# Kernel tuning notes

Hardware: AMD Instinct MI355X
Metric: run time of the kernel (lower is better)

## Reference

```python
import jax, jax.numpy as jnp
import numpy as np
import math

E = 256      # emb_size
H = 4        # num_heads
D = E // H   # head_dim
EXPLORE_SCALE = 0.5
EXPLOIT_SCALE = 0.5
TEMP_MIN = 0.5
TEMP_MAX = 2.0


def setup_inputs() -> dict:
    key = jax.random.key(0)
    ks = jax.random.split(key, 12)
    B, S = 4, 2048
    his_emb = jax.random.normal(ks[0], (B, S, E), dtype=jnp.float32)
    src_key_padding_mask = jax.random.randint(ks[1], (B, S), 0, 2) > 0
    explore = jax.random.uniform(ks[2], (B, S), dtype=jnp.float32)
    exploit = jax.random.uniform(ks[3], (B, S), dtype=jnp.float32)
    scale = 1.0 / math.sqrt(E)
    Wq = jax.random.normal(ks[4], (E, E), dtype=jnp.float32) * scale
    bq = jnp.zeros((E,), dtype=jnp.float32)
    Wk = jax.random.normal(ks[5], (E, E), dtype=jnp.float32) * scale
    bk = jnp.zeros((E,), dtype=jnp.float32)
    Wv = jax.random.normal(ks[6], (E, E), dtype=jnp.float32) * scale
    bv = jnp.zeros((E,), dtype=jnp.float32)
    Wo = jax.random.normal(ks[7], (E, E), dtype=jnp.float32) * scale
    bo = jnp.zeros((E,), dtype=jnp.float32)
    return {"his_emb": his_emb, "src_key_padding_mask": src_key_padding_mask,
            "explore": explore, "exploit": exploit,
            "Wq": Wq, "bq": bq, "Wk": Wk, "bk": bk,
            "Wv": Wv, "bv": bv, "Wo": Wo, "bo": bo}


def reference(his_emb, src_key_padding_mask, explore, exploit,
              Wq, bq, Wk, bk, Wv, bv, Wo, bo):
    B, S, _ = his_emb.shape
    # projections -> [B, H, S, D]
    q = (his_emb @ Wq + bq).reshape(B, S, H, D).transpose(0, 2, 1, 3)
    k = (his_emb @ Wk + bk).reshape(B, S, H, D).transpose(0, 2, 1, 3)
    v = (his_emb @ Wv + bv).reshape(B, S, H, D).transpose(0, 2, 1, 3)
    logits = jnp.einsum('bhqd,bhkd->bhqk', q, k) / math.sqrt(D)
    attn_mask = src_key_padding_mask[:, None, None, :]  # [B,1,1,S] over keys
    logits = jnp.where(attn_mask, -1e16, logits)
    # per-query dynamic temperature
    temp = 1.0 + EXPLORE_SCALE * explore - EXPLOIT_SCALE * exploit  # [B,S]
    temp = jnp.clip(temp, TEMP_MIN, TEMP_MAX)
    temp = jnp.where(src_key_padding_mask, 1.0, temp)
    logits = logits / temp[:, None, :, None]
    probs = jax.nn.softmax(logits, axis=-1)
    probs = jnp.where(attn_mask, 0.0, probs)
    probs = probs / jnp.maximum(probs.sum(axis=-1, keepdims=True), 1e-8)
    out = jnp.einsum('bhqk,bhkd->bhqd', probs, v)
    out = out.transpose(0, 2, 1, 3).reshape(B, S, E)
    out = out @ Wo + bo
    return jnp.where(src_key_padding_mask[:, :, None], 0.0, out)
```

## Files before the change

kernel.cpp:

```cpp
#include <hip/hip_runtime.h>
#include <math.h>

#define B_ 4
#define S_ 2048
#define E_ 256
#define H_ 4
#define D_ 64
#define NROW (B_*S_)
#define NCH 2
#define CHK (S_/NCH)
#define NT (CHK/64)
#define LOG2E 1.4426950408889634f
#define NFM  (-17.312340490667562f)

typedef __attribute__((ext_vector_type(8)))  short short8;
typedef __attribute__((ext_vector_type(4)))  float floatx4;
typedef __attribute__((ext_vector_type(16))) float floatx16;

__device__ __forceinline__ short f2bf(float f){
    union{float f; unsigned u;} x; x.f = f;
    unsigned r = x.u + 0x7fffu + ((x.u>>16)&1u);
    return (short)(r>>16);
}
__device__ __forceinline__ unsigned cvtpk(float a, float b){
    unsigned r; asm("v_cvt_pk_bf16_f32 %0, %1, %2" : "=v"(r) : "v"(a), "v"(b)); return r;
}

__global__ __launch_bounds__(256) void prep(
    const float* __restrict__ W0, const float* __restrict__ W1,
    const float* __restrict__ W2, const float* __restrict__ W3,
    const float* __restrict__ X,
    short* __restrict__ T0, short* __restrict__ T1,
    short* __restrict__ T2, short* __restrict__ T3,
    short* __restrict__ Xb)
{
    __shared__ float L[64][65];
    const int t = threadIdx.x;
    if (blockIdx.x >= 16){
        const int cid = (blockIdx.x - 16) + 128*blockIdx.y;
        const float4* src = (const float4*)(X + (size_t)cid*4096 + t*16);
        short8 o0, o1; float4 u;
        u = src[0]; o0[0]=f2bf(u.x); o0[1]=f2bf(u.y); o0[2]=f2bf(u.z); o0[3]=f2bf(u.w);
        u = src[1]; o0[4]=f2bf(u.x); o0[5]=f2bf(u.y); o0[6]=f2bf(u.z); o0[7]=f2bf(u.w);
        u = src[2]; o1[0]=f2bf(u.x); o1[1]=f2bf(u.y); o1[2]=f2bf(u.z); o1[3]=f2bf(u.w);
        u = src[3]; o1[4]=f2bf(u.x); o1[5]=f2bf(u.y); o1[6]=f2bf(u.z); o1[7]=f2bf(u.w);
        short* dst = Xb + (size_t)cid*4096 + t*16;
        *(short8*)dst = o0; *(short8*)(dst+8) = o1;
        return;
    }
    const float* W = blockIdx.y==0?W0: blockIdx.y==1?W1: blockIdx.y==2?W2:W3;
    short*       T = blockIdx.y==0?T0: blockIdx.y==1?T1: blockIdx.y==2?T2:T3;
    const int k0 = (blockIdx.x>>2)*64, n0 = (blockIdx.x&3)*64;
    {
        int r = t>>2, c0 = (t&3)*16;
        const float4* p = (const float4*)(W + (size_t)(k0+r)*E_ + n0 + c0);
        #pragma unroll
        for (int j=0;j<4;++j){
            float4 u = p[j];
            L[r][c0+4*j]=u.x; L[r][c0+4*j+1]=u.y; L[r][c0+4*j+2]=u.z; L[r][c0+4*j+3]=u.w;
        }
    }
    __syncthreads();
    {
        int n = t>>2, kk0 = (t&3)*16;
        short8 o0, o1;
        #pragma unroll
        for(int j=0;j<8;++j) o0[j] = f2bf(L[kk0+j][n]);
        #pragma unroll
        for(int j=0;j<8;++j) o1[j] = f2bf(L[kk0+8+j][n]);
        short* dst = T + (size_t)(n0+n)*E_ + k0 + kk0;
        *(short8*)dst = o0; *(short8*)(dst+8) = o1;
    }
}

__global__ __launch_bounds__(256) void qkv_gemm(
    const short* __restrict__ Xb,
    const short* __restrict__ Wtq, const float* __restrict__ bq,
    const short* __restrict__ Wtk, const float* __restrict__ bk,
    const short* __restrict__ Wtv, const float* __restrict__ bv,
    short* __restrict__ Q, short* __restrict__ K, short* __restrict__ Vt)
{
    const int z = blockIdx.z;
    const short* Wt   = z==0?Wtq: z==1?Wtk:Wtv;
    const float* bias = z==0?bq:  z==1?bk:bv;

    __shared__ __align__(16) short As[64][72];
    __shared__ __align__(16) short Bs[64][72];

    const int t=threadIdx.x, w=t>>6, lane=t&63, ln=lane&15, quad=lane>>4;
    const int m0 = blockIdx.y*64, n0 = blockIdx.x*64;

    floatx4 acc[4] = {};
    for (int kt=0; kt<E_; kt+=64){
        __syncthreads();
        {
            int r=t>>2, c0=(t&3)*16;
            const uint4* pa = (const uint4*)(Xb + (size_t)(m0+r)*E_ + kt + c0);
            *(uint4*)&As[r][c0] = pa[0]; *(uint4*)&As[r][c0+8] = pa[1];
            const uint4* pb = (const uint4*)(Wt + (size_t)(n0+r)*E_ + kt + c0);
            *(uint4*)&Bs[r][c0] = pb[0]; *(uint4*)&Bs[r][c0+8] = pb[1];
        }
        __syncthreads();
        short8 a0 = *(const short8*)&As[w*16+ln][quad*8];
        short8 a1 = *(const short8*)&As[w*16+ln][32+quad*8];
        #pragma unroll
        for (int c=0;c<4;++c){
            short8 b0 = *(const short8*)&Bs[c*16+ln][quad*8];
            short8 b1 = *(const short8*)&Bs[c*16+ln][32+quad*8];
            acc[c] = __builtin_amdgcn_mfma_f32_16x16x32_bf16(a0,b0,acc[c],0,0,0);
            acc[c] = __builtin_amdgcn_mfma_f32_16x16x32_bf16(a1,b1,acc[c],0,0,0);
        }
    }
    if (z<2){
        short* dst = z==0?Q:K;
        #pragma unroll
        for(int c=0;c<4;++c){
            int colg = n0 + c*16 + ln;
            float bia = bias[colg];
            #pragma unroll
            for(int reg=0;reg<4;++reg){
                int row = m0 + w*16 + quad*4 + reg;
                dst[(size_t)row*E_ + colg] = f2bf(acc[c][reg] + bia);
            }
        }
    } else {
        #pragma unroll
        for(int c=0;c<4;++c){
            int colg = n0 + c*16 + ln;
            int hx = colg>>6, d = colg&63;
            float bia = bias[colg];
            #pragma unroll
            for(int reg=0;reg<4;++reg){
                int row = m0 + w*16 + quad*4 + reg;
                int bb = row>>11, s = row&(S_-1);
                Vt[((size_t)((bb*H_+hx)*D_+d))*S_ + s] = f2bf(acc[c][reg] + bia);
            }
        }
    }
}

__global__ __launch_bounds__(256) void attn_mfma(
    const short* __restrict__ Qb, const short* __restrict__ Kb, const short* __restrict__ Vtb,
    const int* __restrict__ mask,
    const float* __restrict__ explore, const float* __restrict__ exploit,
    float* __restrict__ OP, float* __restrict__ Lb)
{
    const int bid = blockIdx.x + 16*blockIdx.y + 32*blockIdx.z;
    const int swz = (bid & 7)*64 + (bid >> 3);
    const int bx = swz & 15;
    const int ck = (swz >> 4) & 1;
    const int z  = swz >> 5;
    const int b = z >> 2, h = z & 3;
    const int q0 = bx*128;
    const int k0 = ck*CHK;

    const int t = threadIdx.x, w = t>>6, lane = t&63, l31 = lane&31, hi = lane>>5;

    __shared__ __align__(16) short Ks[2][64][72];
    __shared__ __align__(16) short Vs[2][64][72];
    __shared__ float mb[2][64];

    const int qbase = q0 + w*32;
    const int qg = qbase + l31;
    float tsc2;
    {
        float ex = explore[b*S_+qg], xp = exploit[b*S_+qg];
        float tmp = fminf(fmaxf(1.0f + 0.5f*ex - 0.5f*xp, 0.5f), 2.0f);
        if (mask[b*S_+qg]) tmp = 1.0f;
        tsc2 = LOG2E/(tmp*8.0f);
    }
    const size_t qrow = (size_t)(b*S_+qg)*E_ + h*D_ + hi*8;
    const short8 qf0 = *(const short8*)(Qb + qrow);
    const short8 qf1 = *(const short8*)(Qb + qrow + 16);
    const short8 qf2 = *(const short8*)(Qb + qrow + 32);
    const short8 qf3 = *(const short8*)(Qb + qrow + 48);

    floatx16 ofa = {}, ofb = {};
    float lacc = 0.0f;

    const int sr = t>>2, sc = (t&3)*16;
    const short* kgp = Kb  + (size_t)(b*S_)*E_ + h*D_ + sc;
    const short* vgp = Vtb + ((size_t)(b*H_+h)*D_ + sr)*S_;

    uint4 rk0, rk1, rv0, rv1; float mfv = 0.0f;
    {
        const uint4* gk = (const uint4*)(kgp + (size_t)(k0+sr)*E_);
        rk0 = gk[0]; rk1 = gk[1];
        const uint4* gv = (const uint4*)(vgp + k0 + sc);
        rv0 = gv[0]; rv1 = gv[1];
        if (t < 64) mfv = mask[b*S_ + k0 + t] ? -1e30f : NFM;
    }
    *(uint4*)&Ks[0][sr][sc] = rk0; *(uint4*)&Ks[0][sr][sc+8] = rk1;
    *(uint4*)&Vs[0][sr][sc] = rv0; *(uint4*)&Vs[0][sr][sc+8] = rv1;
    if (t < 64) mb[0][t] = mfv;
    {
        const uint4* gk = (const uint4*)(kgp + (size_t)(k0+64+sr)*E_);
        rk0 = gk[0]; rk1 = gk[1];
        const uint4* gv = (const uint4*)(vgp + k0 + 64 + sc);
        rv0 = gv[0]; rv1 = gv[1];
        if (t < 64) mfv = mask[b*S_ + k0 + 64 + t] ? -1e30f : NFM;
    }
    __syncthreads();

    int cur = 0;
    #pragma unroll 1
    for (int it = 0; it < NT; ++it){
        const short (*Kc)[72] = Ks[cur];
        const short (*Vc)[72] = Vs[cur];
        #pragma unroll
        for (int kg = 0; kg < 2; ++kg){
            floatx16 st = {};
            const short8 kf0 = *(const short8*)&Kc[kg*32+l31][hi*8];
            const short8 kf1 = *(const short8*)&Kc[kg*32+l31][16+hi*8];
            const short8 kf2 = *(const short8*)&Kc[kg*32+l31][32+hi*8];
            const short8 kf3 = *(const short8*)&Kc[kg*32+l31][48+hi*8];
            __builtin_amdgcn_s_setprio(1);
            st = __builtin_amdgcn_mfma_f32_32x32x16_bf16(kf0, qf0, st, 0,0,0);
            st = __builtin_amdgcn_mfma_f32_32x32x16_bf16(kf1, qf1, st, 0,0,0);
            st = __builtin_amdgcn_mfma_f32_32x32x16_bf16(kf2, qf2, st, 0,0,0);
            st = __builtin_amdgcn_mfma_f32_32x32x16_bf16(kf3, qf3, st, 0,0,0);
            __builtin_amdgcn_s_setprio(0);
            const float4 m0_ = *(const float4*)&mb[cur][kg*32 +      4*hi];
            const float4 m1_ = *(const float4*)&mb[cur][kg*32 +  8 + 4*hi];
            const float4 m2_ = *(const float4*)&mb[cur][kg*32 + 16 + 4*hi];
            const float4 m3_ = *(const float4*)&mb[cur][kg*32 + 24 + 4*hi];
            const float mbf[16] = {m0_.x,m0_.y,m0_.z,m0_.w, m1_.x,m1_.y,m1_.z,m1_.w,
                                   m2_.x,m2_.y,m2_.z,m2_.w, m3_.x,m3_.y,m3_.z,m3_.w};
            float p[16];
            #pragma unroll
            for (int r = 0; r < 16; ++r){
                p[r] = __builtin_amdgcn_exp2f(st[r]*tsc2 + mbf[r]);
                lacc += p[r];
            }
            #pragma unroll
            for (int c = 0; c < 2; ++c){
                unsigned w0 = cvtpk(p[c*8+0], p[c*8+1]);
                unsigned w1 = cvtpk(p[c*8+2], p[c*8+3]);
                unsigned w2 = cvtpk(p[c*8+4], p[c*8+5]);
                unsigned w3 = cvtpk(p[c*8+6], p[c*8+7]);
                asm("v_permlane32_swap_b32 %0, %1" : "+v"(w0), "+v"(w2));
                asm("v_permlane32_swap_b32 %0, %1" : "+v"(w1), "+v"(w3));
                union { uint4 u; short8 s; } pc;
                pc.u.x = w0; pc.u.y = w1; pc.u.z = w2; pc.u.w = w3;
                const short8 vf0 = *(const short8*)&Vc[l31]   [kg*32 + c*16 + hi*8];
                const short8 vf1 = *(const short8*)&Vc[32+l31][kg*32 + c*16 + hi*8];
                __builtin_amdgcn_s_setprio(1);
                ofa = __builtin_amdgcn_mfma_f32_32x32x16_bf16(pc.s, vf0, ofa, 0,0,0);
                ofb = __builtin_amdgcn_mfma_f32_32x32x16_bf16(pc.s, vf1, ofb, 0,0,0);
                __builtin_amdgcn_s_setprio(0);
            }
        }
        if (it + 1 < NT){
            *(uint4*)&Ks[cur^1][sr][sc] = rk0; *(uint4*)&Ks[cur^1][sr][sc+8] = rk1;
            *(uint4*)&Vs[cur^1][sr][sc] = rv0; *(uint4*)&Vs[cur^1][sr][sc+8] = rv1;
            if (t < 64) mb[cur^1][t] = mfv;
            if (it + 2 < NT){
                const int kt2 = k0 + (it+2)*64;
                const uint4* gk = (const uint4*)(kgp + (size_t)(kt2+sr)*E_);
                rk0 = gk[0]; rk1 = gk[1];
                const uint4* gv = (const uint4*)(vgp + kt2 + sc);
                rv0 = gv[0]; rv1 = gv[1];
                if (t < 64) mfv = mask[b*S_ + kt2 + t] ? -1e30f : NFM;
            }
        }
        __syncthreads();
        cur ^= 1;
    }

    const float l = lacc + __shfl_xor(lacc, 32);
    const size_t obase = ((size_t)(ck*B_+b)*H_+h)*S_;
    if (hi == 0) Lb[obase + qg] = l;
    #pragma unroll
    for (int r = 0; r < 16; ++r){
        const int q = qbase + (r&3) + 8*(r>>2) + 4*hi;
        float* dst = OP + (obase + q)*D_;
        dst[l31]      = ofa[r];
        dst[32 + l31] = ofb[r];
    }
}

__global__ __launch_bounds__(256) void out_gemm(
    const float* __restrict__ OP, const float* __restrict__ Lb,
    const short* __restrict__ Wto, const float* __restrict__ bo,
    const int* __restrict__ mask, float* __restrict__ out)
{
    __shared__ __align__(16) short As[64][72];
    __shared__ __align__(16) short Bs[64][72];
    const int bid = blockIdx.x + 4*blockIdx.y;
    const int swz = (bid & 7)*64 + (bid >> 3);
    const int n0 = (swz & 3)*64;
    const int m0 = (swz >> 2)*64;
    const int t=threadIdx.x, w=t>>6, lane=t&63, ln=lane&15, quad=lane>>4;
    floatx4 acc[4] = {};
    const int sr=t>>2, sc=(t&3)*16;
    const int rowg = m0 + sr, bb = rowg>>11, ss = rowg&(S_-1);
    #pragma unroll 1
    for (int kt=0; kt<E_; kt+=64){
        const int hx = kt>>6;
        const size_t r0 = ((size_t)(bb)*H_+hx)*S_+ss;
        const size_t r1 = ((size_t)(B_+bb)*H_+hx)*S_+ss;
        const float lsum = Lb[r0] + Lb[r1];
        const float rl = 1.0f/fmaxf(lsum, 1e-8f);
        const float* pa0 = OP + r0*D_ + sc;
        const float* pa1 = OP + r1*D_ + sc;
        const float4 u0 = *(const float4*)(pa0+0), u1 = *(const float4*)(pa0+4),
                     u2 = *(const float4*)(pa0+8), u3 = *(const float4*)(pa0+12);
        const float4 v0 = *(const float4*)(pa1+0), v1 = *(const float4*)(pa1+4),
                     v2 = *(const float4*)(pa1+8), v3 = *(const float4*)(pa1+12);
        const uint4* pb = (const uint4*)(Wto + (size_t)(n0+sr)*E_ + kt + sc);
        const uint4 bw0 = pb[0], bw1 = pb[1];
        __syncthreads();
        union { uint4 u; short8 s; } cA, cB;
        cA.u.x = cvtpk((u0.x+v0.x)*rl, (u0.y+v0.y)*rl);
        cA.u.y = cvtpk((u0.z+v0.z)*rl, (u0.w+v0.w)*rl);
        cA.u.z = cvtpk((u1.x+v1.x)*rl, (u1.y+v1.y)*rl);
        cA.u.w = cvtpk((u1.z+v1.z)*rl, (u1.w+v1.w)*rl);
        cB.u.x = cvtpk((u2.x+v2.x)*rl, (u2.y+v2.y)*rl);
        cB.u.y = cvtpk((u2.z+v2.z)*rl, (u2.w+v2.w)*rl);
        cB.u.z = cvtpk((u3.x+v3.x)*rl, (u3.y+v3.y)*rl);
        cB.u.w = cvtpk((u3.z+v3.z)*rl, (u3.w+v3.w)*rl);
        *(short8*)&As[sr][sc]   = cA.s;
        *(short8*)&As[sr][sc+8] = cB.s;
        *(uint4*)&Bs[sr][sc] = bw0; *(uint4*)&Bs[sr][sc+8] = bw1;
        __syncthreads();
        const short8 a0 = *(const short8*)&As[w*16+ln][quad*8];
        const short8 a1 = *(const short8*)&As[w*16+ln][32+quad*8];
        #pragma unroll
        for (int c=0;c<4;++c){
            const short8 b0 = *(const short8*)&Bs[c*16+ln][quad*8];
            const short8 b1 = *(const short8*)&Bs[c*16+ln][32+quad*8];
            acc[c] = __builtin_amdgcn_mfma_f32_16x16x32_bf16(a0,b0,acc[c],0,0,0);
            acc[c] = __builtin_amdgcn_mfma_f32_16x16x32_bf16(a1,b1,acc[c],0,0,0);
        }
    }
    #pragma unroll
    for(int c=0;c<4;++c){
        const int colg = n0 + c*16 + ln;
        const float bia = bo[colg];
        #pragma unroll
        for(int reg=0;reg<4;++reg){
            const int row = m0 + w*16 + quad*4 + reg;
            out[(size_t)row*E_ + colg] = mask[row] ? 0.0f : (acc[c][reg] + bia);
        }
    }
}

extern "C" void kernel_launch(void* const* d_in, const int* in_sizes, int n_in,
                              void* d_out, int out_size, void* d_ws, size_t ws_size,
                              hipStream_t stream) {
    const float* his     = (const float*)d_in[0];
    const int*   mask    = (const int*)d_in[1];
    const float* explore = (const float*)d_in[2];
    const float* exploit = (const float*)d_in[3];
    const float* Wq = (const float*)d_in[4];
    const float* bq = (const float*)d_in[5];
    const float* Wk = (const float*)d_in[6];
    const float* bk = (const float*)d_in[7];
    const float* Wv = (const float*)d_in[8];
    const float* bv = (const float*)d_in[9];
    const float* Wo = (const float*)d_in[10];
    const float* bo = (const float*)d_in[11];

    char* ws = (char*)d_ws;
    const size_t NE2 = (size_t)NROW * E_ * 2;
    short* Wtq  = (short*)(ws);                    ws += E_*E_*2;
    short* Wtk  = (short*)(ws);                    ws += E_*E_*2;
    short* Wtv  = (short*)(ws);                    ws += E_*E_*2;
    short* Wto  = (short*)(ws);                    ws += E_*E_*2;
    short* Xb   = (short*)(ws);                    ws += NE2;
    short* Qb   = (short*)(ws);                    ws += NE2;
    short* Kb   = (short*)(ws);                    ws += NE2;
    short* Vtb  = (short*)(ws);                    ws += NE2;
    float* OP   = (float*)(ws);                    ws += (size_t)NCH*NROW*E_*4;
    float* Lb   = (float*)(ws);                    ws += (size_t)NCH*B_*H_*S_*4;

    prep<<<dim3(144,4), 256, 0, stream>>>(Wq, Wk, Wv, Wo, his, Wtq, Wtk, Wtv, Wto, Xb);

    qkv_gemm<<<dim3(E_/64, NROW/64, 3), 256, 0, stream>>>(
        Xb, Wtq, bq, Wtk, bk, Wtv, bv, Qb, Kb, Vtb);

    attn_mfma<<<dim3(S_/128, NCH, B_*H_), 256, 0, stream>>>(
        Qb, Kb, Vtb, mask, explore, exploit, OP, Lb);

    out_gemm<<<dim3(E_/64, NROW/64), 256, 0, stream>>>(OP, Lb, Wto, bo, mask, (float*)d_out);
}
```

Baseline: 132.2 us.

## Split attention keys into four chunks and fuse X bf16 conversion into QKV GEMM

The key dimension of attention is split into four chunks instead of two, doubling the number of attention blocks. The goal is better occupancy across the GPU's compute units, and the block swizzle and out_gemm reduction are generalized to match. The standalone fp32-to-bf16 conversion of X is removed from the prep kernel, and qkv_gemm now converts while loading tiles. This saves a kernel pass and the Xb round trip, at the cost of more partial-output traffic and reduction work in out_gemm, and X is now read and converted three times (once per z slice).

```diff
diff --git a/kernel.cpp b/kernel.cpp
--- a/kernel.cpp
+++ b/kernel.cpp
@@ -7,7 +7,7 @@
 #define H_ 4
 #define D_ 64
 #define NROW (B_*S_)
-#define NCH 2
+#define NCH 4
 #define CHK (S_/NCH)
 #define NT (CHK/64)
 #define LOG2E 1.4426950408889634f
@@ -26,30 +26,16 @@
     unsigned r; asm("v_cvt_pk_bf16_f32 %0, %1, %2" : "=v"(r) : "v"(a), "v"(b)); return r;
 }
 
-__global__ __launch_bounds__(256) void prep(
+__global__ __launch_bounds__(256) void prep_w(
     const float* __restrict__ W0, const float* __restrict__ W1,
     const float* __restrict__ W2, const float* __restrict__ W3,
-    const float* __restrict__ X,
     short* __restrict__ T0, short* __restrict__ T1,
-    short* __restrict__ T2, short* __restrict__ T3,
-    short* __restrict__ Xb)
+    short* __restrict__ T2, short* __restrict__ T3)
 {
+    const float* W = blockIdx.y==0?W0: blockIdx.y==1?W1: blockIdx.y==2?W2:W3;
+    short*       T = blockIdx.y==0?T0: blockIdx.y==1?T1: blockIdx.y==2?T2:T3;
     __shared__ float L[64][65];
     const int t = threadIdx.x;
-    if (blockIdx.x >= 16){
-        const int cid = (blockIdx.x - 16) + 128*blockIdx.y;
-        const float4* src = (const float4*)(X + (size_t)cid*4096 + t*16);
-        short8 o0, o1; float4 u;
-        u = src[0]; o0[0]=f2bf(u.x); o0[1]=f2bf(u.y); o0[2]=f2bf(u.z); o0[3]=f2bf(u.w);
-        u = src[1]; o0[4]=f2bf(u.x); o0[5]=f2bf(u.y); o0[6]=f2bf(u.z); o0[7]=f2bf(u.w);
-        u = src[2]; o1[0]=f2bf(u.x); o1[1]=f2bf(u.y); o1[2]=f2bf(u.z); o1[3]=f2bf(u.w);
-        u = src[3]; o1[4]=f2bf(u.x); o1[5]=f2bf(u.y); o1[6]=f2bf(u.z); o1[7]=f2bf(u.w);
-        short* dst = Xb + (size_t)cid*4096 + t*16;
-        *(short8*)dst = o0; *(short8*)(dst+8) = o1;
-        return;
-    }
-    const float* W = blockIdx.y==0?W0: blockIdx.y==1?W1: blockIdx.y==2?W2:W3;
-    short*       T = blockIdx.y==0?T0: blockIdx.y==1?T1: blockIdx.y==2?T2:T3;
     const int k0 = (blockIdx.x>>2)*64, n0 = (blockIdx.x&3)*64;
     {
         int r = t>>2, c0 = (t&3)*16;
@@ -74,7 +60,7 @@
 }
 
 __global__ __launch_bounds__(256) void qkv_gemm(
-    const short* __restrict__ Xb,
+    const float* __restrict__ X,
     const short* __restrict__ Wtq, const float* __restrict__ bq,
     const short* __restrict__ Wtk, const float* __restrict__ bk,
     const short* __restrict__ Wtv, const float* __restrict__ bv,
@@ -95,8 +81,14 @@
         __syncthreads();
         {
             int r=t>>2, c0=(t&3)*16;
-            const uint4* pa = (const uint4*)(Xb + (size_t)(m0+r)*E_ + kt + c0);
-            *(uint4*)&As[r][c0] = pa[0]; *(uint4*)&As[r][c0+8] = pa[1];
+            const float4* pa = (const float4*)(X + (size_t)(m0+r)*E_ + kt + c0);
+            short8 s0, s1;
+            float4 u;
+            u=pa[0]; s0[0]=f2bf(u.x); s0[1]=f2bf(u.y); s0[2]=f2bf(u.z); s0[3]=f2bf(u.w);
+            u=pa[1]; s0[4]=f2bf(u.x); s0[5]=f2bf(u.y); s0[6]=f2bf(u.z); s0[7]=f2bf(u.w);
+            u=pa[2]; s1[0]=f2bf(u.x); s1[1]=f2bf(u.y); s1[2]=f2bf(u.z); s1[3]=f2bf(u.w);
+            u=pa[3]; s1[4]=f2bf(u.x); s1[5]=f2bf(u.y); s1[6]=f2bf(u.z); s1[7]=f2bf(u.w);
+            *(short8*)&As[r][c0] = s0; *(short8*)&As[r][c0+8] = s1;
             const uint4* pb = (const uint4*)(Wt + (size_t)(n0+r)*E_ + kt + c0);
             *(uint4*)&Bs[r][c0] = pb[0]; *(uint4*)&Bs[r][c0+8] = pb[1];
         }
@@ -145,11 +137,11 @@
     const float* __restrict__ explore, const float* __restrict__ exploit,
     float* __restrict__ OP, float* __restrict__ Lb)
 {
-    const int bid = blockIdx.x + 16*blockIdx.y + 32*blockIdx.z;
-    const int swz = (bid & 7)*64 + (bid >> 3);
+    const int bid = blockIdx.x + 16*blockIdx.y + 16*NCH*blockIdx.z;
+    const int swz = (bid & 7)*128 + (bid >> 3);
     const int bx = swz & 15;
-    const int ck = (swz >> 4) & 1;
-    const int z  = swz >> 5;
+    const int ck = (swz >> 4) & (NCH-1);
+    const int z  = swz >> 6;
     const int b = z >> 2, h = z & 3;
     const int q0 = bx*128;
     const int k0 = ck*CHK;
@@ -226,22 +218,22 @@
             const float4 m3_ = *(const float4*)&mb[cur][kg*32 + 24 + 4*hi];
             const float mbf[16] = {m0_.x,m0_.y,m0_.z,m0_.w, m1_.x,m1_.y,m1_.z,m1_.w,
                                    m2_.x,m2_.y,m2_.z,m2_.w, m3_.x,m3_.y,m3_.z,m3_.w};
-            float p[16];
+            float pr[16];
             #pragma unroll
             for (int r = 0; r < 16; ++r){
-                p[r] = __builtin_amdgcn_exp2f(st[r]*tsc2 + mbf[r]);
-                lacc += p[r];
+                pr[r] = __builtin_amdgcn_exp2f(st[r]*tsc2 + mbf[r]);
+                lacc += pr[r];
             }
             #pragma unroll
             for (int c = 0; c < 2; ++c){
-                unsigned w0 = cvtpk(p[c*8+0], p[c*8+1]);
-                unsigned w1 = cvtpk(p[c*8+2], p[c*8+3]);
-                unsigned w2 = cvtpk(p[c*8+4], p[c*8+5]);
-                unsigned w3 = cvtpk(p[c*8+6], p[c*8+7]);
-                asm("v_permlane32_swap_b32 %0, %1" : "+v"(w0), "+v"(w2));
-                asm("v_permlane32_swap_b32 %0, %1" : "+v"(w1), "+v"(w3));
+                unsigned u0 = cvtpk(pr[c*8+0], pr[c*8+1]);
+                unsigned u1 = cvtpk(pr[c*8+2], pr[c*8+3]);
+                unsigned u2 = cvtpk(pr[c*8+4], pr[c*8+5]);
+                unsigned u3 = cvtpk(pr[c*8+6], pr[c*8+7]);
+                asm("v_permlane32_swap_b32 %0, %1" : "+v"(u0), "+v"(u2));
+                asm("v_permlane32_swap_b32 %0, %1" : "+v"(u1), "+v"(u3));
                 union { uint4 u; short8 s; } pc;
-                pc.u.x = w0; pc.u.y = w1; pc.u.z = w2; pc.u.w = w3;
+                pc.u.x = u0; pc.u.y = u1; pc.u.z = u2; pc.u.w = u3;
                 const short8 vf0 = *(const short8*)&Vc[l31]   [kg*32 + c*16 + hi*8];
                 const short8 vf1 = *(const short8*)&Vc[32+l31][kg*32 + c*16 + hi*8];
                 __builtin_amdgcn_s_setprio(1);
@@ -297,28 +289,33 @@
     #pragma unroll 1
     for (int kt=0; kt<E_; kt+=64){
         const int hx = kt>>6;
-        const size_t r0 = ((size_t)(bb)*H_+hx)*S_+ss;
-        const size_t r1 = ((size_t)(B_+bb)*H_+hx)*S_+ss;
-        const float lsum = Lb[r0] + Lb[r1];
+        float lsum = 0.0f;
+        float4 A0={0,0,0,0}, A1={0,0,0,0}, A2={0,0,0,0}, A3={0,0,0,0};
+        #pragma unroll
+        for (int c=0;c<NCH;++c){
+            const size_t rr = ((size_t)(c*B_+bb)*H_+hx)*S_+ss;
+            lsum += Lb[rr];
+            const float* pa = OP + rr*D_ + sc;
+            const float4 x0=*(const float4*)(pa+0), x1=*(const float4*)(pa+4),
+                         x2=*(const float4*)(pa+8), x3=*(const float4*)(pa+12);
+            A0.x+=x0.x; A0.y+=x0.y; A0.z+=x0.z; A0.w+=x0.w;
+            A1.x+=x1.x; A1.y+=x1.y; A1.z+=x1.z; A1.w+=x1.w;
+            A2.x+=x2.x; A2.y+=x2.y; A2.z+=x2.z; A2.w+=x2.w;
+            A3.x+=x3.x; A3.y+=x3.y; A3.z+=x3.z; A3.w+=x3.w;
+        }
         const float rl = 1.0f/fmaxf(lsum, 1e-8f);
-        const float* pa0 = OP + r0*D_ + sc;
-        const float* pa1 = OP + r1*D_ + sc;
-        const float4 u0 = *(const float4*)(pa0+0), u1 = *(const float4*)(pa0+4),
-                     u2 = *(const float4*)(pa0+8), u3 = *(const float4*)(pa0+12);
-        const float4 v0 = *(const float4*)(pa1+0), v1 = *(const float4*)(pa1+4),
-                     v2 = *(const float4*)(pa1+8), v3 = *(const float4*)(pa1+12);
         const uint4* pb = (const uint4*)(Wto + (size_t)(n0+sr)*E_ + kt + sc);
         const uint4 bw0 = pb[0], bw1 = pb[1];
         __syncthreads();
         union { uint4 u; short8 s; } cA, cB;
-        cA.u.x = cvtpk((u0.x+v0.x)*rl, (u0.y+v0.y)*rl);
-        cA.u.y = cvtpk((u0.z+v0.z)*rl, (u0.w+v0.w)*rl);
-        cA.u.z = cvtpk((u1.x+v1.x)*rl, (u1.y+v1.y)*rl);
-        cA.u.w = cvtpk((u1.z+v1.z)*rl, (u1.w+v1.w)*rl);
-        cB.u.x = cvtpk((u2.x+v2.x)*rl, (u2.y+v2.y)*rl);
-        cB.u.y = cvtpk((u2.z+v2.z)*rl, (u2.w+v2.w)*rl);
-        cB.u.z = cvtpk((u3.x+v3.x)*rl, (u3.y+v3.y)*rl);
-        cB.u.w = cvtpk((u3.z+v3.z)*rl, (u3.w+v3.w)*rl);
+        cA.u.x = cvtpk(A0.x*rl, A0.y*rl);
+        cA.u.y = cvtpk(A0.z*rl, A0.w*rl);
+        cA.u.z = cvtpk(A1.x*rl, A1.y*rl);
+        cA.u.w = cvtpk(A1.z*rl, A1.w*rl);
+        cB.u.x = cvtpk(A2.x*rl, A2.y*rl);
+        cB.u.y = cvtpk(A2.z*rl, A2.w*rl);
+        cB.u.z = cvtpk(A3.x*rl, A3.y*rl);
+        cB.u.w = cvtpk(A3.z*rl, A3.w*rl);
         *(short8*)&As[sr][sc]   = cA.s;
         *(short8*)&As[sr][sc+8] = cB.s;
         *(uint4*)&Bs[sr][sc] = bw0; *(uint4*)&Bs[sr][sc+8] = bw1;
@@ -367,17 +364,16 @@
     short* Wtk  = (short*)(ws);                    ws += E_*E_*2;
     short* Wtv  = (short*)(ws);                    ws += E_*E_*2;
     short* Wto  = (short*)(ws);                    ws += E_*E_*2;
-    short* Xb   = (short*)(ws);                    ws += NE2;
     short* Qb   = (short*)(ws);                    ws += NE2;
     short* Kb   = (short*)(ws);                    ws += NE2;
     short* Vtb  = (short*)(ws);                    ws += NE2;
     float* OP   = (float*)(ws);                    ws += (size_t)NCH*NROW*E_*4;
     float* Lb   = (float*)(ws);                    ws += (size_t)NCH*B_*H_*S_*4;
 
-    prep<<<dim3(144,4), 256, 0, stream>>>(Wq, Wk, Wv, Wo, his, Wtq, Wtk, Wtv, Wto, Xb);
+    prep_w<<<dim3(16,4), 256, 0, stream>>>(Wq, Wk, Wv, Wo, Wtq, Wtk, Wtv, Wto);
 
     qkv_gemm<<<dim3(E_/64, NROW/64, 3), 256, 0, stream>>>(
-        Xb, Wtq, bq, Wtk, bk, Wtv, bv, Qb, Kb, Vtb);
+        his, Wtq, bq, Wtk, bk, Wtv, bv, Qb, Kb, Vtb);
 
     attn_mfma<<<dim3(S_/128, NCH, B_*H_), 256, 0, stream>>>(
         Qb, Kb, Vtb, mask, explore, exploit, OP, Lb);
```

Result: slower. 143.2 us (+8.3%).
